# Kernel tuning notes

Hardware: AMD Instinct MI355X
Metric: run time of the kernel (lower is better)

Reference implementation:

```python
import jax, jax.numpy as jnp
import numpy as np

D_MODEL = 1024
N_HEADS = 16
D_HEAD = D_MODEL // N_HEADS
BLOCK = 128
B, T = 2, 2048


def setup_inputs() -> dict:
    key = jax.random.key(0)
    ks = jax.random.split(key, 5)
    x = jax.random.normal(ks[0], (B, T, D_MODEL), dtype=jnp.float32)
    def init_w(k):
        # nn.Linear default init scale ~ 1/sqrt(fan_in)
        return jax.random.normal(k, (D_MODEL, D_MODEL), dtype=jnp.float32) / np.sqrt(D_MODEL).astype(np.float32)
    return {
        "x": x,
        "Wq": init_w(ks[1]),
        "Wk": init_w(ks[2]),
        "Wv": init_w(ks[3]),
        "Wo": init_w(ks[4]),
    }


def _flash_attention(Q, K, V, block_size, scale):
    """Online-softmax tiled attention over kv blocks (causal). Q,K,V: (B,H,T,d)."""
    Bb, H, Tt, d = Q.shape
    n_blocks = Tt // block_size
    # (n_blocks, B, H, block, d) so scan streams kv tiles
    Kb = K.reshape(Bb, H, n_blocks, block_size, d).transpose(2, 0, 1, 3, 4)
    Vb = V.reshape(Bb, H, n_blocks, block_size, d).transpose(2, 0, 1, 3, 4)
    starts = jnp.arange(n_blocks) * block_size
    q_pos = jnp.arange(Tt)

    def step(carry, xs):
        m, l, acc = carry
        kb, vb, st = xs
        # scores: (B,H,T,block)
        scores = scale * jnp.einsum('bhtd,bhsd->bhts', Q, kb)
        kv_pos = st + jnp.arange(block_size)
        future = kv_pos[None, :] > q_pos[:, None]          # (T, block)
        scores = jnp.where(future[None, None], -jnp.inf, scores)
        m_new = jnp.maximum(m, jnp.max(scores, axis=-1, keepdims=True))
        p = jnp.exp(scores - m_new)
        corr = jnp.exp(m - m_new)
        l = corr * l + jnp.sum(p, axis=-1, keepdims=True)
        acc = corr * acc + jnp.einsum('bhts,bhsd->bhtd', p, vb)
        return (m_new, l, acc), None

    m0 = jnp.full((Bb, H, Tt, 1), -jnp.inf, dtype=jnp.float32)
    l0 = jnp.zeros((Bb, H, Tt, 1), dtype=jnp.float32)
    a0 = jnp.zeros((Bb, H, Tt, d), dtype=jnp.float32)
    (m, l, acc), _ = jax.lax.scan(step, (m0, l0, a0), (Kb, Vb, starts))
    return acc / jnp.maximum(l, 1e-12)


def reference(x, Wq, Wk, Wv, Wo):
    Bx, Tx, _ = x.shape
    scale = 1.0 / np.sqrt(D_HEAD).astype(np.float32)
    def proj(W):  # nn.Linear: y = x @ W.T
        y = jnp.einsum('btm,nm->btn', x, W)
        return y.reshape(Bx, Tx, N_HEADS, D_HEAD).transpose(0, 2, 1, 3)
    Q, K, V = proj(Wq), proj(Wk), proj(Wv)
    O = _flash_attention(Q.astype(jnp.float32), K.astype(jnp.float32), V.astype(jnp.float32), BLOCK, scale)
    O = O.astype(x.dtype).transpose(0, 2, 1, 3).reshape(Bx, Tx, D_MODEL)
    return jnp.einsum('btm,nm->btn', O, Wo)
```

## Files before the change

kernel.cpp:

```cpp
#include <hip/hip_runtime.h>
#include <hip/hip_bf16.h>

typedef __attribute__((ext_vector_type(8))) short short8;
typedef __attribute__((ext_vector_type(4))) float f32x4;
typedef __attribute__((ext_vector_type(2))) unsigned int uint2v;
typedef __attribute__((ext_vector_type(4))) unsigned int uint4v;
typedef unsigned short u16;

#define MFMA_BF16(a, b, c) __builtin_amdgcn_mfma_f32_16x16x32_bf16(a, b, c, 0, 0, 0)

#define T_SEQ 2048
#define DMODEL 1024
#define NHEADS 16
#define DHEAD 64
#define NEG_BIG (-30000.0f)
#define QSCALE 0.1803368801111f

#if __has_builtin(__builtin_amdgcn_exp2f)
#define EXP2(x) __builtin_amdgcn_exp2f(x)
#else
#define EXP2(x) exp2f(x)
#endif

__device__ __forceinline__ unsigned bfr(unsigned u) {
  return (u + 0x7fffu + ((u >> 16) & 1u)) >> 16;
}
__device__ __forceinline__ uint4v ld8bf(const float* __restrict__ p) {
  const uint4v a = *(const uint4v*)p;
  const uint4v b = *(const uint4v*)(p + 4);
  uint4v r;
  r[0] = bfr(a[0]) | (bfr(a[1]) << 16);
  r[1] = bfr(a[2]) | (bfr(a[3]) << 16);
  r[2] = bfr(b[0]) | (bfr(b[1]) << 16);
  r[3] = bfr(b[2]) | (bfr(b[3]) << 16);
  return r;
}
__device__ __forceinline__ u16 f2bf(float f) {
  unsigned u = __float_as_uint(f);
  u += 0x7fffu + ((u >> 16) & 1u);
  return (u16)(u >> 16);
}
__device__ __forceinline__ void gld16(const u16* g, u16* l) {
  __builtin_amdgcn_global_load_lds(
      (const __attribute__((address_space(1))) unsigned int*)g,
      (__attribute__((address_space(3))) unsigned int*)l, 16, 0, 0);
}

__global__ __launch_bounds__(256) void cvt_all(
    const float* __restrict__ x, const float* __restrict__ wq,
    const float* __restrict__ wk, const float* __restrict__ wv,
    const float* __restrict__ wo, u16* __restrict__ xh, u16* __restrict__ wqh,
    u16* __restrict__ wkh, u16* __restrict__ wvh, u16* __restrict__ woh) {
  int bi = blockIdx.x;
  const float* s;
  u16* d;
  size_t base;
  if (bi < 2048) {
    s = x; d = xh; base = (size_t)bi * 2048;
  } else {
    int k = (bi - 2048) >> 9;
    int r = (bi - 2048) & 511;
    s = (k == 0) ? wq : (k == 1) ? wk : (k == 2) ? wv : wo;
    d = (k == 0) ? wqh : (k == 1) ? wkh : (k == 2) ? wvh : woh;
    base = (size_t)r * 2048;
  }
  size_t i = base + (size_t)threadIdx.x * 8;
  *(uint4v*)&d[i] = ld8bf(&s[i]);
}

__global__ __launch_bounds__(256) void gemm_qkv(
    const u16* __restrict__ X, const u16* __restrict__ Wq,
    const u16* __restrict__ Wk, const u16* __restrict__ Wv,
    u16* __restrict__ Qo, u16* __restrict__ Ko, u16* __restrict__ Vo) {
  __shared__ __attribute__((aligned(16))) u16 As[128 * 32];
  __shared__ __attribute__((aligned(16))) u16 Bs[128 * 32];
  const int tid = threadIdx.x, lane = tid & 63, w = tid >> 6;
  const int wm = (w >> 1) * 64, wn = (w & 1) * 64;
  const int lrow = lane & 15;
  const int lk = (lane >> 4) << 3;
  const int lq = (lane >> 4) << 2;
  const int mBase = blockIdx.x * 128, nBase = blockIdx.y * 128;
  const u16* Bt = (blockIdx.z == 0) ? Wq : (blockIdx.z == 1) ? Wk : Wv;
  u16* D = (blockIdx.z == 0) ? Qo : (blockIdx.z == 1) ? Ko : Vo;
  const float scale = (blockIdx.z == 0) ? QSCALE : 1.0f;

  f32x4 acc[4][4];
#pragma unroll
  for (int mi = 0; mi < 4; mi++)
#pragma unroll
    for (int ni = 0; ni < 4; ni++) acc[mi][ni] = (f32x4)0.0f;

  for (int k0 = 0; k0 < 1024; k0 += 32) {
    __syncthreads();
#pragma unroll
    for (int i = 0; i < 2; i++) {
      int c = i * 256 + tid;
      int r = c >> 2, kk = (c & 3) << 3;
      gld16(&X[(size_t)(mBase + r) * 1024 + k0 + kk], &As[c * 8]);
      gld16(&Bt[(size_t)(nBase + r) * 1024 + k0 + kk], &Bs[c * 8]);
    }
    __syncthreads();
    short8 af[4], bf[4];
#pragma unroll
    for (int mi = 0; mi < 4; mi++)
      af[mi] = *(const short8*)&As[(wm + mi * 16 + lrow) * 32 + lk];
#pragma unroll
    for (int ni = 0; ni < 4; ni++)
      bf[ni] = *(const short8*)&Bs[(wn + ni * 16 + lrow) * 32 + lk];
#pragma unroll
    for (int mi = 0; mi < 4; mi++)
#pragma unroll
      for (int ni = 0; ni < 4; ni++)
        acc[mi][ni] = MFMA_BF16(af[mi], bf[ni], acc[mi][ni]);
  }
  const int vz = (blockIdx.z == 2);
#pragma unroll
  for (int mi = 0; mi < 4; mi++)
#pragma unroll
    for (int r = 0; r < 4; r++) {
      int m = mBase + wm + mi * 16 + lq + r;
      int b = m >> 11, t = m & 2047;
#pragma unroll
      for (int ni = 0; ni < 4; ni++) {
        int n = nBase + wn + ni * 16 + lrow;
        int h = n >> 6, dd = n & 63;
        size_t idx = vz ? (((size_t)((b * NHEADS + h) * DHEAD + dd)) * T_SEQ + t)
                        : ((((size_t)(b * NHEADS + h)) * T_SEQ + t) * DHEAD + dd);
        D[idx] = f2bf(acc[mi][ni][r] * scale);
      }
    }
}

__global__ __launch_bounds__(256) void attn_snake(
    const u16* __restrict__ Qg, const u16* __restrict__ Kg,
    const u16* __restrict__ Vtg, u16* __restrict__ Ob) {
  __shared__ __attribute__((aligned(16))) u16 smem[13824];
  u16* Qs = smem;
  u16* Ps = smem;
  u16* Ks = smem + 4608;
  u16* Vt = smem + 9216;

  const int tid = threadIdx.x;
  const int w = tid >> 6, lane = tid & 63;
  const int lrow = lane & 15;
  const int quad = lane >> 4;
  const int lk = quad << 3;
  const int q_local = w * 16 + lrow;

  const int j = blockIdx.x;
  const int bh = blockIdx.y;
  const int b = bh >> 4, h = bh & 15;
  const u16* Qp = Qg + (size_t)bh * T_SEQ * DHEAD;
  const u16* Kp = Kg + (size_t)bh * T_SEQ * DHEAD;
  const u16* Vp = Vtg + (size_t)bh * DHEAD * T_SEQ;

#pragma unroll
  for (int p = 0; p < 2; p++) {
    const int qt = p ? (31 - j) : j;
    const int qb = qt * 64;

    __syncthreads();
#pragma unroll
    for (int i = 0; i < 2; i++) {
      int c = i * 256 + tid;
      int r = c >> 3, kk = (c & 7) << 3;
      *(uint4v*)&Qs[r * 72 + kk] =
          *(const uint4v*)&Qp[(size_t)(qb + r) * DHEAD + kk];
    }
    __syncthreads();
    short8 qf[2];
#pragma unroll
    for (int ks = 0; ks < 2; ks++)
      qf[ks] = *(const short8*)&Qs[q_local * 72 + ks * 32 + lk];

    float mst = NEG_BIG, lst = 0.f;
    f32x4 oacc[4];
#pragma unroll
    for (int nd = 0; nd < 4; nd++) oacc[nd] = (f32x4)0.0f;

    const int ntiles = qt + 1;
    for (int kt = 0; kt < ntiles; kt++) {
      const int kvb = kt * 64;
      __syncthreads();
#pragma unroll
      for (int i = 0; i < 2; i++) {
        int c = i * 256 + tid;
        int r = c >> 3, kk = (c & 7) << 3;
        *(uint4v*)&Ks[r * 72 + kk] =
            *(const uint4v*)&Kp[(size_t)(kvb + r) * DHEAD + kk];
        *(uint4v*)&Vt[r * 72 + kk] =
            *(const uint4v*)&Vp[(size_t)r * T_SEQ + kvb + kk];
      }
      __syncthreads();

      f32x4 s[4];
#pragma unroll
      for (int kvt = 0; kvt < 4; kvt++) {
        f32x4 a = (f32x4)0.0f;
#pragma unroll
        for (int ks = 0; ks < 2; ks++) {
          short8 kf = *(const short8*)&Ks[(kvt * 16 + lrow) * 72 + ks * 32 + lk];
          a = MFMA_BF16(kf, qf[ks], a);
        }
        s[kvt] = a;
      }

      if (kt == qt) {
#pragma unroll
        for (int kvt = 0; kvt < 4; kvt++)
#pragma unroll
          for (int r = 0; r < 4; r++)
            if (kvt * 16 + quad * 4 + r > q_local) s[kvt][r] = NEG_BIG;
      }

      float mx = s[0][0];
#pragma unroll
      for (int kvt = 0; kvt < 4; kvt++)
#pragma unroll
        for (int r = 0; r < 4; r++) mx = fmaxf(mx, s[kvt][r]);
      mx = fmaxf(mx, __shfl_xor(mx, 16));
      mx = fmaxf(mx, __shfl_xor(mx, 32));
      float mn = fmaxf(mst, mx);
      float corr = EXP2(mst - mn);
      mst = mn;
      float ls = 0.f;
#pragma unroll
      for (int kvt = 0; kvt < 4; kvt++)
#pragma unroll
        for (int r = 0; r < 4; r++) {
          float pv = EXP2(s[kvt][r] - mn);
          s[kvt][r] = pv;
          ls += pv;
        }
      ls += __shfl_xor(ls, 16);
      ls += __shfl_xor(ls, 32);
      lst = corr * lst + ls;
#pragma unroll
      for (int nd = 0; nd < 4; nd++) oacc[nd] *= corr;

#pragma unroll
      for (int kvt = 0; kvt < 4; kvt++) {
        uint2v pk;
        pk[0] = (__float_as_uint(s[kvt][0]) >> 16) |
                (__float_as_uint(s[kvt][1]) & 0xffff0000u);
        pk[1] = (__float_as_uint(s[kvt][2]) >> 16) |
                (__float_as_uint(s[kvt][3]) & 0xffff0000u);
        *(uint2v*)&Ps[q_local * 72 + kvt * 16 + quad * 4] = pk;
      }

#pragma unroll
      for (int ks = 0; ks < 2; ks++) {
        short8 pf = *(const short8*)&Ps[q_local * 72 + ks * 32 + lk];
#pragma unroll
        for (int nd = 0; nd < 4; nd++) {
          short8 vf = *(const short8*)&Vt[(nd * 16 + lrow) * 72 + ks * 32 + lk];
          oacc[nd] = MFMA_BF16(vf, pf, oacc[nd]);
        }
      }
    }

    float inv = 1.f / lst;
    size_t rowbase = ((size_t)(b * T_SEQ + qb + q_local)) * DMODEL + h * DHEAD;
#pragma unroll
    for (int nd = 0; nd < 4; nd++) {
      uint2v pk;
      pk[0] = (unsigned)f2bf(oacc[nd][0] * inv) |
              ((unsigned)f2bf(oacc[nd][1] * inv) << 16);
      pk[1] = (unsigned)f2bf(oacc[nd][2] * inv) |
              ((unsigned)f2bf(oacc[nd][3] * inv) << 16);
      *(uint2v*)&Ob[rowbase + nd * 16 + quad * 4] = pk;
    }
  }
}

__global__ __launch_bounds__(256) void gemm_out_bf(const u16* __restrict__ O,
                                                   const u16* __restrict__ Wo,
                                                   float* __restrict__ Out) {
  __shared__ __attribute__((aligned(16))) u16 As[128 * 32];
  __shared__ __attribute__((aligned(16))) u16 Bs[128 * 32];
  const int tid = threadIdx.x, lane = tid & 63, w = tid >> 6;
  const int wm = (w >> 1) * 64, wn = (w & 1) * 64;
  const int lrow = lane & 15;
  const int lk = (lane >> 4) << 3;
  const int lq = (lane >> 4) << 2;
  const int mBase = blockIdx.x * 128, nBase = blockIdx.y * 128;

  f32x4 acc[4][4];
#pragma unroll
  for (int mi = 0; mi < 4; mi++)
#pragma unroll
    for (int ni = 0; ni < 4; ni++) acc[mi][ni] = (f32x4)0.0f;

  for (int k0 = 0; k0 < 1024; k0 += 32) {
    __syncthreads();
#pragma unroll
    for (int i = 0; i < 2; i++) {
      int c = i * 256 + tid;
      int r = c >> 2, kk = (c & 3) << 3;
      gld16(&O[(size_t)(mBase + r) * 1024 + k0 + kk], &As[c * 8]);
      gld16(&Wo[(size_t)(nBase + r) * 1024 + k0 + kk], &Bs[c * 8]);
    }
    __syncthreads();
    short8 af[4], bf[4];
#pragma unroll
    for (int mi = 0; mi < 4; mi++)
      af[mi] = *(const short8*)&As[(wm + mi * 16 + lrow) * 32 + lk];
#pragma unroll
    for (int ni = 0; ni < 4; ni++)
      bf[ni] = *(const short8*)&Bs[(wn + ni * 16 + lrow) * 32 + lk];
#pragma unroll
    for (int mi = 0; mi < 4; mi++)
#pragma unroll
      for (int ni = 0; ni < 4; ni++)
        acc[mi][ni] = MFMA_BF16(af[mi], bf[ni], acc[mi][ni]);
  }
#pragma unroll
  for (int mi = 0; mi < 4; mi++)
#pragma unroll
    for (int r = 0; r < 4; r++) {
      int m = mBase + wm + mi * 16 + lq + r;
#pragma unroll
      for (int ni = 0; ni < 4; ni++)
        Out[(size_t)m * DMODEL + nBase + wn + ni * 16 + lrow] = acc[mi][ni][r];
    }
}

extern "C" void kernel_launch(void* const* d_in, const int* in_sizes, int n_in,
                              void* d_out, int out_size, void* d_ws,
                              size_t ws_size, hipStream_t stream) {
  const float* x = (const float*)d_in[0];
  const float* Wq = (const float*)d_in[1];
  const float* Wk = (const float*)d_in[2];
  const float* Wv = (const float*)d_in[3];
  const float* Wo = (const float*)d_in[4];
  float* out = (float*)d_out;

  u16* xh = (u16*)d_ws;
  u16* wqh = xh + 4194304;
  u16* wkh = wqh + 1048576;
  u16* wvh = wkh + 1048576;
  u16* woh = wvh + 1048576;
  u16* Q = woh + 1048576;
  u16* K = Q + 4194304;
  u16* V = K + 4194304;
  u16* O = V + 4194304;

  cvt_all<<<dim3(4096), 256, 0, stream>>>(x, Wq, Wk, Wv, Wo, xh, wqh, wkh, wvh, woh);
  gemm_qkv<<<dim3(32, 8, 3), 256, 0, stream>>>(xh, wqh, wkh, wvh, Q, K, V);
  attn_snake<<<dim3(16, 32), 256, 0, stream>>>(Q, K, V, O);
  gemm_out_bf<<<dim3(32, 8), 256, 0, stream>>>(O, woh, out);
}
```

Before: 197.0 us.

## Double-buffer GEMM and attention LDS tiles, swizzle KV, add lazy softmax rescale

Both GEMMs and the attention kernel now double-buffer their LDS tiles, prefetching the next K-slice or KV tile with direct global-to-LDS loads while the current one is computed, and use one barrier per iteration instead of two. The attention K/V tiles drop the padded 72-stride layout for an XOR-swizzled 64-stride layout to avoid LDS bank conflicts. Online softmax only rescales the accumulator when the wave-wide max grows by more than a threshold. s_setprio hints are placed around the MFMA sections. This costs more LDS per block, which may reduce occupancy, and the lazy rescale lets exponent values run up to 2^8 before renormalising.

```diff
diff --git a/kernel.cpp b/kernel.cpp
--- a/kernel.cpp
+++ b/kernel.cpp
@@ -15,6 +15,7 @@
 #define DHEAD 64
 #define NEG_BIG (-30000.0f)
 #define QSCALE 0.1803368801111f
+#define RESCALE_THR 8.0f
 
 #if __has_builtin(__builtin_amdgcn_exp2f)
 #define EXP2(x) __builtin_amdgcn_exp2f(x)
@@ -72,8 +73,8 @@
     const u16* __restrict__ X, const u16* __restrict__ Wq,
     const u16* __restrict__ Wk, const u16* __restrict__ Wv,
     u16* __restrict__ Qo, u16* __restrict__ Ko, u16* __restrict__ Vo) {
-  __shared__ __attribute__((aligned(16))) u16 As[128 * 32];
-  __shared__ __attribute__((aligned(16))) u16 Bs[128 * 32];
+  __shared__ __attribute__((aligned(16))) u16 As[2][128 * 32];
+  __shared__ __attribute__((aligned(16))) u16 Bs[2][128 * 32];
   const int tid = threadIdx.x, lane = tid & 63, w = tid >> 6;
   const int wm = (w >> 1) * 64, wn = (w & 1) * 64;
   const int lrow = lane & 15;
@@ -90,28 +91,35 @@
 #pragma unroll
     for (int ni = 0; ni < 4; ni++) acc[mi][ni] = (f32x4)0.0f;
 
-  for (int k0 = 0; k0 < 1024; k0 += 32) {
-    __syncthreads();
+  auto stage = [&](int buf, int k0) {
 #pragma unroll
     for (int i = 0; i < 2; i++) {
       int c = i * 256 + tid;
       int r = c >> 2, kk = (c & 3) << 3;
-      gld16(&X[(size_t)(mBase + r) * 1024 + k0 + kk], &As[c * 8]);
-      gld16(&Bt[(size_t)(nBase + r) * 1024 + k0 + kk], &Bs[c * 8]);
-    }
-    __syncthreads();
+      gld16(&X[(size_t)(mBase + r) * 1024 + k0 + kk], &As[buf][c * 8]);
+      gld16(&Bt[(size_t)(nBase + r) * 1024 + k0 + kk], &Bs[buf][c * 8]);
+    }
+  };
+
+  stage(0, 0);
+  __syncthreads();
+  int cur = 0;
+  for (int k0 = 0; k0 < 1024; k0 += 32) {
+    if (k0 + 32 < 1024) stage(cur ^ 1, k0 + 32);
     short8 af[4], bf[4];
 #pragma unroll
     for (int mi = 0; mi < 4; mi++)
-      af[mi] = *(const short8*)&As[(wm + mi * 16 + lrow) * 32 + lk];
+      af[mi] = *(const short8*)&As[cur][(wm + mi * 16 + lrow) * 32 + lk];
 #pragma unroll
     for (int ni = 0; ni < 4; ni++)
-      bf[ni] = *(const short8*)&Bs[(wn + ni * 16 + lrow) * 32 + lk];
+      bf[ni] = *(const short8*)&Bs[cur][(wn + ni * 16 + lrow) * 32 + lk];
 #pragma unroll
     for (int mi = 0; mi < 4; mi++)
 #pragma unroll
       for (int ni = 0; ni < 4; ni++)
         acc[mi][ni] = MFMA_BF16(af[mi], bf[ni], acc[mi][ni]);
+    __syncthreads();
+    cur ^= 1;
   }
   const int vz = (blockIdx.z == 2);
 #pragma unroll
@@ -134,17 +142,16 @@
 __global__ __launch_bounds__(256) void attn_snake(
     const u16* __restrict__ Qg, const u16* __restrict__ Kg,
     const u16* __restrict__ Vtg, u16* __restrict__ Ob) {
-  __shared__ __attribute__((aligned(16))) u16 smem[13824];
+  __shared__ __attribute__((aligned(16))) u16 smem[20992];
   u16* Qs = smem;
   u16* Ps = smem;
-  u16* Ks = smem + 4608;
-  u16* Vt = smem + 9216;
 
   const int tid = threadIdx.x;
   const int w = tid >> 6, lane = tid & 63;
   const int lrow = lane & 15;
   const int quad = lane >> 4;
   const int lk = quad << 3;
+  const int rsw = lrow & 7;
   const int q_local = w * 16 + lrow;
 
   const int j = blockIdx.x;
@@ -154,6 +161,17 @@
   const u16* Kp = Kg + (size_t)bh * T_SEQ * DHEAD;
   const u16* Vp = Vtg + (size_t)bh * DHEAD * T_SEQ;
 
+  auto stage_kv = [&](u16* Ksd, u16* Vtd, int kvb) {
+#pragma unroll
+    for (int i = 0; i < 2; i++) {
+      int c = i * 256 + tid;
+      int r = c >> 3;
+      int sw = ((c & 7) ^ (r & 7)) << 3;
+      gld16(&Kp[(size_t)(kvb + r) * DHEAD + sw], &Ksd[c * 8]);
+      gld16(&Vp[(size_t)r * T_SEQ + kvb + sw], &Vtd[c * 8]);
+    }
+  };
+
 #pragma unroll
   for (int p = 0; p < 2; p++) {
     const int qt = p ? (31 - j) : j;
@@ -167,7 +185,9 @@
       *(uint4v*)&Qs[r * 72 + kk] =
           *(const uint4v*)&Qp[(size_t)(qb + r) * DHEAD + kk];
     }
+    stage_kv(smem + 4608, smem + 12800, 0);
     __syncthreads();
+
     short8 qf[2];
 #pragma unroll
     for (int ks = 0; ks < 2; ks++)
@@ -179,31 +199,28 @@
     for (int nd = 0; nd < 4; nd++) oacc[nd] = (f32x4)0.0f;
 
     const int ntiles = qt + 1;
+    int cur = 0;
     for (int kt = 0; kt < ntiles; kt++) {
-      const int kvb = kt * 64;
-      __syncthreads();
-#pragma unroll
-      for (int i = 0; i < 2; i++) {
-        int c = i * 256 + tid;
-        int r = c >> 3, kk = (c & 7) << 3;
-        *(uint4v*)&Ks[r * 72 + kk] =
-            *(const uint4v*)&Kp[(size_t)(kvb + r) * DHEAD + kk];
-        *(uint4v*)&Vt[r * 72 + kk] =
-            *(const uint4v*)&Vp[(size_t)r * T_SEQ + kvb + kk];
-      }
-      __syncthreads();
+      u16* Ksc = smem + 4608 + cur * 4096;
+      u16* Vtc = smem + 12800 + cur * 4096;
+      if (kt + 1 < ntiles)
+        stage_kv(smem + 4608 + (cur ^ 1) * 4096,
+                 smem + 12800 + (cur ^ 1) * 4096, (kt + 1) * 64);
 
       f32x4 s[4];
+      __builtin_amdgcn_s_setprio(1);
 #pragma unroll
       for (int kvt = 0; kvt < 4; kvt++) {
         f32x4 a = (f32x4)0.0f;
 #pragma unroll
         for (int ks = 0; ks < 2; ks++) {
-          short8 kf = *(const short8*)&Ks[(kvt * 16 + lrow) * 72 + ks * 32 + lk];
+          short8 kf = *(const short8*)&Ksc[(kvt * 16 + lrow) * 64 +
+                                           ((((ks << 2) + quad) ^ rsw) << 3)];
           a = MFMA_BF16(kf, qf[ks], a);
         }
         s[kvt] = a;
       }
+      __builtin_amdgcn_s_setprio(0);
 
       if (kt == qt) {
 #pragma unroll
@@ -220,23 +237,26 @@
         for (int r = 0; r < 4; r++) mx = fmaxf(mx, s[kvt][r]);
       mx = fmaxf(mx, __shfl_xor(mx, 16));
       mx = fmaxf(mx, __shfl_xor(mx, 32));
-      float mn = fmaxf(mst, mx);
-      float corr = EXP2(mst - mn);
-      mst = mn;
+      if (!__all(mx <= mst + RESCALE_THR)) {
+        float mn = fmaxf(mst, mx);
+        float corr = EXP2(mst - mn);
+        mst = mn;
+        lst *= corr;
+#pragma unroll
+        for (int nd = 0; nd < 4; nd++) oacc[nd] *= corr;
+      }
       float ls = 0.f;
 #pragma unroll
       for (int kvt = 0; kvt < 4; kvt++)
 #pragma unroll
         for (int r = 0; r < 4; r++) {
-          float pv = EXP2(s[kvt][r] - mn);
+          float pv = EXP2(s[kvt][r] - mst);
           s[kvt][r] = pv;
           ls += pv;
         }
       ls += __shfl_xor(ls, 16);
       ls += __shfl_xor(ls, 32);
-      lst = corr * lst + ls;
-#pragma unroll
-      for (int nd = 0; nd < 4; nd++) oacc[nd] *= corr;
+      lst += ls;
 
 #pragma unroll
       for (int kvt = 0; kvt < 4; kvt++) {
@@ -248,15 +268,21 @@
         *(uint2v*)&Ps[q_local * 72 + kvt * 16 + quad * 4] = pk;
       }
 
+      __builtin_amdgcn_s_setprio(1);
 #pragma unroll
       for (int ks = 0; ks < 2; ks++) {
         short8 pf = *(const short8*)&Ps[q_local * 72 + ks * 32 + lk];
 #pragma unroll
         for (int nd = 0; nd < 4; nd++) {
-          short8 vf = *(const short8*)&Vt[(nd * 16 + lrow) * 72 + ks * 32 + lk];
+          short8 vf = *(const short8*)&Vtc[(nd * 16 + lrow) * 64 +
+                                           ((((ks << 2) + quad) ^ rsw) << 3)];
           oacc[nd] = MFMA_BF16(vf, pf, oacc[nd]);
         }
       }
+      __builtin_amdgcn_s_setprio(0);
+
+      __syncthreads();
+      cur ^= 1;
     }
 
     float inv = 1.f / lst;
@@ -276,8 +302,8 @@
 __global__ __launch_bounds__(256) void gemm_out_bf(const u16* __restrict__ O,
                                                    const u16* __restrict__ Wo,
                                                    float* __restrict__ Out) {
-  __shared__ __attribute__((aligned(16))) u16 As[128 * 32];
-  __shared__ __attribute__((aligned(16))) u16 Bs[128 * 32];
+  __shared__ __attribute__((aligned(16))) u16 As[2][128 * 32];
+  __shared__ __attribute__((aligned(16))) u16 Bs[2][128 * 32];
   const int tid = threadIdx.x, lane = tid & 63, w = tid >> 6;
   const int wm = (w >> 1) * 64, wn = (w & 1) * 64;
   const int lrow = lane & 15;
@@ -291,28 +317,35 @@
 #pragma unroll
     for (int ni = 0; ni < 4; ni++) acc[mi][ni] = (f32x4)0.0f;
 
-  for (int k0 = 0; k0 < 1024; k0 += 32) {
-    __syncthreads();
+  auto stage = [&](int buf, int k0) {
 #pragma unroll
     for (int i = 0; i < 2; i++) {
       int c = i * 256 + tid;
       int r = c >> 2, kk = (c & 3) << 3;
-      gld16(&O[(size_t)(mBase + r) * 1024 + k0 + kk], &As[c * 8]);
-      gld16(&Wo[(size_t)(nBase + r) * 1024 + k0 + kk], &Bs[c * 8]);
-    }
-    __syncthreads();
+      gld16(&O[(size_t)(mBase + r) * 1024 + k0 + kk], &As[buf][c * 8]);
+      gld16(&Wo[(size_t)(nBase + r) * 1024 + k0 + kk], &Bs[buf][c * 8]);
+    }
+  };
+
+  stage(0, 0);
+  __syncthreads();
+  int cur = 0;
+  for (int k0 = 0; k0 < 1024; k0 += 32) {
+    if (k0 + 32 < 1024) stage(cur ^ 1, k0 + 32);
     short8 af[4], bf[4];
 #pragma unroll
     for (int mi = 0; mi < 4; mi++)
-      af[mi] = *(const short8*)&As[(wm + mi * 16 + lrow) * 32 + lk];
+      af[mi] = *(const short8*)&As[cur][(wm + mi * 16 + lrow) * 32 + lk];
 #pragma unroll
     for (int ni = 0; ni < 4; ni++)
-      bf[ni] = *(const short8*)&Bs[(wn + ni * 16 + lrow) * 32 + lk];
+      bf[ni] = *(const short8*)&Bs[cur][(wn + ni * 16 + lrow) * 32 + lk];
 #pragma unroll
     for (int mi = 0; mi < 4; mi++)
 #pragma unroll
       for (int ni = 0; ni < 4; ni++)
         acc[mi][ni] = MFMA_BF16(af[mi], bf[ni], acc[mi][ni]);
+    __syncthreads();
+    cur ^= 1;
   }
 #pragma unroll
   for (int mi = 0; mi < 4; mi++)
```

Measured after the change: 186.8 us. -5.2%, faster.
